# Optimization experiments

Hardware: AMD Instinct MI355X
Metric: run time of the kernel (lower is better)

The kernel has to match this reference:

```python
import jax, jax.numpy as jnp
import numpy as np
from jax import lax


def setup_inputs() -> dict:
    key = jax.random.key(0)
    ks = jax.random.split(key, 3)
    N, Cin, Cout, H, W = 4, 256, 256, 96, 96
    x = jax.random.normal(ks[0], (N, Cin, H, W), jnp.float32)
    # DCNv2-style internal offset/mask conv: 27 = 9 dy + 9 dx + 9 mask logits
    w_off = jax.random.normal(ks[1], (27, Cin, 3, 3), jnp.float32) * 0.01
    b_off = jnp.zeros((27,), jnp.float32)
    w = jax.random.normal(ks[2], (Cout, Cin, 3, 3), jnp.float32) * (1.0 / np.sqrt(Cin * 9))
    b = jnp.zeros((Cout,), jnp.float32)
    gamma = jnp.ones((Cout,), jnp.float32)
    beta = jnp.zeros((Cout,), jnp.float32)
    return {"x": x, "w_off": w_off, "b_off": b_off, "w": w, "b": b, "gamma": gamma, "beta": beta}


def _bilinear(img, py, px):
    # img: [C,H,W]; py,px: [K,H,W] float sampling coords. Zero outside bounds.
    C, H, W = img.shape
    flat = img.reshape(C, -1)
    y0 = jnp.floor(py)
    x0 = jnp.floor(px)
    ly = py - y0
    lx = px - x0

    def gather(yc, xc):
        valid = (yc >= 0) & (yc <= H - 1) & (xc >= 0) & (xc <= W - 1)
        yi = jnp.clip(yc, 0, H - 1).astype(jnp.int32)
        xi = jnp.clip(xc, 0, W - 1).astype(jnp.int32)
        idx = (yi * W + xi).reshape(-1)
        v = flat[:, idx].reshape((C,) + yc.shape)  # [C,K,H,W]
        return v * valid.astype(img.dtype)

    v00 = gather(y0, x0)
    v01 = gather(y0, x0 + 1)
    v10 = gather(y0 + 1, x0)
    v11 = gather(y0 + 1, x0 + 1)
    return (v00 * (1 - ly) * (1 - lx) + v01 * (1 - ly) * lx
            + v10 * ly * (1 - lx) + v11 * ly * lx)


def _forward(x, w_off, b_off, w, b, gamma, beta):
    N, C, H, W = x.shape
    Cout = w.shape[0]
    dn = ("NCHW", "OIHW", "NCHW")
    # internal offset/mask conv (3x3, stride 1, pad 1)
    om = lax.conv_general_dilated(x, w_off, (1, 1), [(1, 1), (1, 1)], dimension_numbers=dn)
    om = om + b_off[None, :, None, None]
    dy, dx, m = om[:, :9], om[:, 9:18], jax.nn.sigmoid(om[:, 18:])
    # base 3x3 kernel grid, dilation 1, padding 1 (centered taps -1..1)
    ky, kx = jnp.meshgrid(jnp.arange(3) - 1, jnp.arange(3) - 1, indexing="ij")
    py = dy + jnp.arange(H, dtype=x.dtype)[None, None, :, None] + ky.reshape(1, 9, 1, 1).astype(x.dtype)
    px = dx + jnp.arange(W, dtype=x.dtype)[None, None, None, :] + kx.reshape(1, 9, 1, 1).astype(x.dtype)
    sampled = jax.vmap(_bilinear)(x, py, px)  # [N,C,9,H,W]
    sampled = sampled * m[:, None]            # DCNv2 modulation mask
    y = jnp.einsum("nckhw,ock->nohw", sampled, w.reshape(Cout, C, 9))
    y = y + b[None, :, None, None]
    # BatchNorm2d (training-mode batch statistics) + ReLU
    mean = y.mean(axis=(0, 2, 3))
    var = y.var(axis=(0, 2, 3))
    y = (y - mean[None, :, None, None]) * lax.rsqrt(var[None, :, None, None] + 1e-5)
    y = y * gamma[None, :, None, None] + beta[None, :, None, None]
    return jax.nn.relu(y)


def reference(x, w_off, b_off, w, b, gamma, beta):
    return _forward(x, w_off, b_off, w, b, gamma, beta)
```

## Files before the change

### kernel.cpp

```cpp
#include <hip/hip_runtime.h>
#include <cmath>

#define H 96
#define W 96
#define HW 9216
#define CIN 256
#define COUT 256
#define NB 4
#define NCH 72
#define NGR 36
#define NIV 18

typedef float f32x4 __attribute__((ext_vector_type(4)));
typedef float f32x2 __attribute__((ext_vector_type(2)));
typedef short bf16x8 __attribute__((ext_vector_type(8)));

__device__ __forceinline__ unsigned short f2bf(float f) {
  unsigned int u = __float_as_uint(f);
  u += 0x7fff + ((u >> 16) & 1);
  return (unsigned short)(u >> 16);
}
__device__ __forceinline__ float bf2f(unsigned short u) {
  return __uint_as_float(((unsigned int)u) << 16);
}
__device__ __forceinline__ f32x2 up2(unsigned int u) {
  f32x2 r;
  r.x = __uint_as_float(u << 16);
  r.y = __uint_as_float(u & 0xffff0000u);
  return r;
}
__device__ __forceinline__ unsigned int cvtpk(float lo, float hi) {
  unsigned int r;
  asm("v_cvt_pk_bf16_f32 %0, %1, %2" : "=v"(r) : "v"(lo), "v"(hi));
  return r;
}

__device__ __forceinline__ void bar() {
  asm volatile("s_waitcnt lgkmcnt(0)" ::: "memory");
  __builtin_amdgcn_s_barrier();
  asm volatile("" ::: "memory");
}

__global__ __launch_bounds__(256)
void xt_convert(const float* __restrict__ x, unsigned short* __restrict__ xT) {
  __shared__ unsigned short ls[64][72];
  int tid = threadIdx.x;
  int hwbase = blockIdx.x * 64;
  int cbase  = blockIdx.y * 64;
  int n      = blockIdx.z;

  {
    int cl = tid >> 2, qd = tid & 3;
    const float* src = x + ((size_t)(n * CIN + cbase + cl)) * HW + hwbase + qd * 16;
#pragma unroll
    for (int m = 0; m < 4; ++m) {
      float4 v = *(const float4*)(src + m * 4);
      int hwl = qd * 16 + m * 4;
      ls[hwl + 0][cl] = f2bf(v.x);
      ls[hwl + 1][cl] = f2bf(v.y);
      ls[hwl + 2][cl] = f2bf(v.z);
      ls[hwl + 3][cl] = f2bf(v.w);
    }
  }
  __syncthreads();
  {
    int hw = tid >> 2, part = tid & 3;
    unsigned short* dst = xT + ((size_t)(n * HW + hwbase + hw)) * CIN + cbase + part * 16;
    *(uint4*)(dst + 0) = *(const uint4*)(&ls[hw][part * 16 + 0]);
    *(uint4*)(dst + 8) = *(const uint4*)(&ls[hw][part * 16 + 8]);
  }
}

__global__ __launch_bounds__(256)
void wa_convert(const float* __restrict__ w, unsigned short* __restrict__ Ag) {
  int gid = blockIdx.x * 256 + threadIdx.x;
  int ch = gid >> 10;
  int rest = gid & 1023;
  int ot = rest >> 6, l = rest & 63;
  int o = ot * 16 + (l & 15);
  int k = ch >> 3, cc = ch & 7;
  int cbase = cc * 32 + (l >> 4) * 8;
  unsigned short r[8];
#pragma unroll
  for (int j = 0; j < 8; ++j)
    r[j] = f2bf(w[((size_t)o * CIN + cbase + j) * 9 + k]);
  uint4 pk;
  pk.x = (unsigned int)r[0] | ((unsigned int)r[1] << 16);
  pk.y = (unsigned int)r[2] | ((unsigned int)r[3] << 16);
  pk.z = (unsigned int)r[4] | ((unsigned int)r[5] << 16);
  pk.w = (unsigned int)r[6] | ((unsigned int)r[7] << 16);
  *(uint4*)(Ag + (size_t)gid * 8) = pk;
}

__global__ __launch_bounds__(256)
void wa2_convert(const float* __restrict__ w_off, unsigned short* __restrict__ Ag2) {
  int gid = blockIdx.x * 256 + threadIdx.x;
  int ch = gid >> 7;
  int rest = gid & 127;
  int ot = rest >> 6, l = rest & 63;
  int o = ot * 16 + (l & 15);
  int k = ch >> 3, cc = ch & 7;
  int cbase = cc * 32 + (l >> 4) * 8;
  unsigned short r[8];
#pragma unroll
  for (int j = 0; j < 8; ++j)
    r[j] = (o < 27) ? f2bf(w_off[((size_t)o * CIN + cbase + j) * 9 + k]) : (unsigned short)0;
  uint4 pk;
  pk.x = (unsigned int)r[0] | ((unsigned int)r[1] << 16);
  pk.y = (unsigned int)r[2] | ((unsigned int)r[3] << 16);
  pk.z = (unsigned int)r[4] | ((unsigned int)r[5] << 16);
  pk.w = (unsigned int)r[6] | ((unsigned int)r[7] << 16);
  *(uint4*)(Ag2 + (size_t)gid * 8) = pk;
}

__global__ __launch_bounds__(256, 4)
void offset_gemm(const unsigned short* __restrict__ xT,
                 const unsigned short* __restrict__ Ag2,
                 const float* __restrict__ b_off,
                 float* __restrict__ py, float* __restrict__ px,
                 float* __restrict__ mk) {
  __shared__ int sPos[9][64];
  __shared__ unsigned short sB[2][2][4096];

  int tid = threadIdx.x;
  int wv = tid >> 6, lane = tid & 63, quad = lane >> 4, l16 = lane & 15;
  int pixBase = blockIdx.x * 64;
  int n = blockIdx.y;
  const unsigned short* xTn = xT + (size_t)n * HW * CIN;

  if (tid < 64) {
    int hwp = pixBase + tid;
    int hh = hwp / W, wx = hwp % W;
#pragma unroll
    for (int ty = 0; ty < 3; ++ty) {
#pragma unroll
      for (int tx = 0; tx < 3; ++tx) {
        int iy = hh + ty - 1, ix = wx + tx - 1;
        bool ok = (iy >= 0) && (iy < H) && (ix >= 0) && (ix < W);
        sPos[ty * 3 + tx][tid] = ok ? (iy * W + ix) : -1;
      }
    }
  }
  bar();

  int pix0 = tid >> 3, ck0 = tid & 7;
  int pix1 = 32 + (tid >> 3);
  int a0 = (ck0 >> 2) * 2048 + (pix0 >> 4) * 512 + ((ck0 & 3) * 16 + ((pix0 & 15) ^ (ck0 & 3))) * 8;
  int a1 = (ck0 >> 2) * 2048 + (pix1 >> 4) * 512 + ((ck0 & 3) * 16 + ((pix1 & 15) ^ (ck0 & 3))) * 8;

  f32x4 acc[2];
  acc[0] = (f32x4){0.f, 0.f, 0.f, 0.f};
  acc[1] = (f32x4){0.f, 0.f, 0.f, 0.f};

  uint4 dA[2], dB[2];
  auto issue = [&](int g, uint4* d) {
    int k = g % 9, c2 = g / 9;
    int p0 = sPos[k][pix0], p1 = sPos[k][pix1];
    d[0] = (uint4){0, 0, 0, 0};
    d[1] = (uint4){0, 0, 0, 0};
    if (p0 >= 0) d[0] = *(const uint4*)(xTn + (size_t)p0 * CIN + c2 * 64 + ck0 * 8);
    if (p1 >= 0) d[1] = *(const uint4*)(xTn + (size_t)p1 * CIN + c2 * 64 + ck0 * 8);
  };

  bf16x8 afr[4];
  auto aload = [&](int g) {
    int k = g % 9, c2 = g / 9;
    int ch = k * 8 + c2 * 2;
#pragma unroll
    for (int s = 0; s < 2; ++s)
#pragma unroll
      for (int ot = 0; ot < 2; ++ot)
        afr[s * 2 + ot] = *(const bf16x8*)(Ag2 + ((size_t)((ch + s) * 2 + ot) * 64 + lane) * 8);
  };

  int rdAddr0 = wv * 512 + (quad * 16 + (l16 ^ quad)) * 8;
  auto mfmaPhase = [&](int buf, int half) {
    const unsigned short* base = &sB[buf][half][0];
    __builtin_amdgcn_s_setprio(1);
#pragma unroll
    for (int s = 0; s < 2; ++s) {
      bf16x8 bfr = *(const bf16x8*)(base + s * 2048 + rdAddr0);
      acc[0] = __builtin_amdgcn_mfma_f32_16x16x32_bf16(afr[s * 2 + 0], bfr, acc[0], 0, 0, 0);
      acc[1] = __builtin_amdgcn_mfma_f32_16x16x32_bf16(afr[s * 2 + 1], bfr, acc[1], 0, 0, 0);
    }
    __builtin_amdgcn_s_setprio(0);
  };
  auto store = [&](uint4* d, int buf, int half) {
    *(uint4*)(&sB[buf][half][a0]) = d[0];
    *(uint4*)(&sB[buf][half][a1]) = d[1];
  };

  issue(0, dA);
  issue(1, dB);
  aload(0);
  store(dA, 0, 0);
  issue(2, dA);
  store(dB, 0, 1);
  issue(3, dB);
  bar();

  for (int i = 0; i < NIV; ++i) {
    int buf = i & 1;
    mfmaPhase(buf, 0);
    aload(2 * i + 1);
    if (i < NIV - 1) store(dA, buf ^ 1, 0);
    if (i < NIV - 2) issue(2 * i + 4, dA);
    mfmaPhase(buf, 1);
    if (i < NIV - 1) store(dB, buf ^ 1, 1);
    if (i < NIV - 2) issue(2 * i + 5, dB);
    if (i < NIV - 1) aload(2 * i + 2);
    bar();
  }

  int pix = pixBase + wv * 16 + l16;
  int he = pix / W, we = pix % W;
#pragma unroll
  for (int ot = 0; ot < 2; ++ot) {
#pragma unroll
    for (int r = 0; r < 4; ++r) {
      int kk = ot * 16 + quad * 4 + r;
      if (kk >= 27) continue;
      float v = acc[ot][r] + b_off[kk];
      if (kk < 9) {
        py[(size_t)(n * 9 + kk) * HW + pix] = v + (float)he + (float)(kk / 3 - 1);
      } else if (kk < 18) {
        int j = kk - 9;
        px[(size_t)(n * 9 + j) * HW + pix] = v + (float)we + (float)(j % 3 - 1);
      } else {
        mk[(size_t)(n * 9 + (kk - 18)) * HW + pix] = 1.f / (1.f + expf(-v));
      }
    }
  }
}

__global__ __launch_bounds__(512, 4)
void fused_gemm(const unsigned short* __restrict__ xT,
                const unsigned short* __restrict__ Ag,
                const float* __restrict__ py,
                const float* __restrict__ px,
                const float* __restrict__ mk,
                unsigned short* __restrict__ yb,
                float* __restrict__ sumArr, float* __restrict__ sqArr) {
  __shared__ int   sIdx4[9][64][4];
  __shared__ float sWgt4[9][64][4];
  __shared__ unsigned short sB[2][2][4096];

  int tid = threadIdx.x;
  int wv = tid >> 6, lane = tid & 63, quad = lane >> 4, l16 = lane & 15;
  int pixBase = blockIdx.x * 64;
  int n = blockIdx.y;
  const unsigned short* xTn = xT + (size_t)n * HW * CIN;

  {
    int pix0 = tid & 63;
    int k0 = tid >> 6;
#pragma unroll
    for (int rep = 0; rep < 2; ++rep) {
      int k = (rep == 0) ? k0 : 8;
      if (rep == 1 && tid >= 64) break;
      int off = (n * 9 + k) * HW + pixBase + pix0;
      float fy = py[off], fx = px[off], fm = mk[off];
      float y0f = floorf(fy), x0f = floorf(fx);
      float ly = fy - y0f, lx = fx - x0f;
      int y0 = (int)y0f, x0 = (int)x0f;
      int cy0 = min(max(y0, 0), H - 1), cy1 = min(max(y0 + 1, 0), H - 1);
      int cx0 = min(max(x0, 0), W - 1), cx1 = min(max(x0 + 1, 0), W - 1);
      float vy0 = (y0 >= 0 && y0 <= H - 1) ? 1.f : 0.f;
      float vy1 = (y0 + 1 >= 0 && y0 + 1 <= H - 1) ? 1.f : 0.f;
      float vx0 = (x0 >= 0 && x0 <= W - 1) ? 1.f : 0.f;
      float vx1 = (x0 + 1 >= 0 && x0 + 1 <= W - 1) ? 1.f : 0.f;
      int4 iv;
      iv.x = cy0 * W + cx0;
      iv.y = cy0 * W + cx1;
      iv.z = cy1 * W + cx0;
      iv.w = cy1 * W + cx1;
      float4 wf;
      wf.x = (1.f - ly) * (1.f - lx) * fm * vy0 * vx0;
      wf.y = (1.f - ly) * lx * fm * vy0 * vx1;
      wf.z = ly * (1.f - lx) * fm * vy1 * vx0;
      wf.w = ly * lx * fm * vy1 * vx1;
      *(int4*)(&sIdx4[k][pix0][0]) = iv;
      *(float4*)(&sWgt4[k][pix0][0]) = wf;
    }
  }
  bar();

  int pixS  = ((wv & 3) << 4) | (lane >> 2);
  int qS    = lane & 3;
  int chunk = ((wv >> 2) << 2) | qS;
  int co    = chunk * 8;
  int sAddr = (chunk >> 2) * 2048 + (wv & 3) * 512 + (qS * 16 + ((lane >> 2) ^ qS)) * 8;

  f32x4 acc[2][4];
#pragma unroll
  for (int i = 0; i < 2; ++i)
#pragma unroll
    for (int pt = 0; pt < 4; ++pt) acc[i][pt] = (f32x4){0.f, 0.f, 0.f, 0.f};

  uint4 cnA[4], cnB[4];
  float wgA[4], wgB[4];
  auto issue = [&](int g, uint4* cn, float* wt) {
    int k = g % 9, c2 = g / 9;
    int4 iv = *(const int4*)(&sIdx4[k][pixS][0]);
    float4 wf = *(const float4*)(&sWgt4[k][pixS][0]);
    int coff = c2 * 64 + co;
    cn[0] = *(const uint4*)(xTn + (size_t)iv.x * CIN + coff);
    cn[1] = *(const uint4*)(xTn + (size_t)iv.y * CIN + coff);
    cn[2] = *(const uint4*)(xTn + (size_t)iv.z * CIN + coff);
    cn[3] = *(const uint4*)(xTn + (size_t)iv.w * CIN + coff);
    wt[0] = wf.x; wt[1] = wf.y; wt[2] = wf.z; wt[3] = wf.w;
  };

  auto blendOne = [&](unsigned int u0, unsigned int u1, unsigned int u2,
                      unsigned int u3, const float* wt) -> unsigned int {
    f32x2 s = up2(u0) * wt[0];
    s += up2(u1) * wt[1];
    s += up2(u2) * wt[2];
    s += up2(u3) * wt[3];
    return cvtpk(s.x, s.y);
  };
  auto blendStore = [&](uint4* cn, const float* wt, int buf, int half) {
    uint4 r;
    r.x = blendOne(cn[0].x, cn[1].x, cn[2].x, cn[3].x, wt);
    r.y = blendOne(cn[0].y, cn[1].y, cn[2].y, cn[3].y, wt);
    r.z = blendOne(cn[0].z, cn[1].z, cn[2].z, cn[3].z, wt);
    r.w = blendOne(cn[0].w, cn[1].w, cn[2].w, cn[3].w, wt);
    *(uint4*)(&sB[buf][half][sAddr]) = r;
  };

  bf16x8 afr[4];
  auto aload = [&](int g) {
    int k = g % 9, c2 = g / 9;
    int ch = k * 8 + c2 * 2;
#pragma unroll
    for (int s = 0; s < 2; ++s)
#pragma unroll
      for (int ot = 0; ot < 2; ++ot)
        afr[s * 2 + ot] = *(const bf16x8*)(Ag + ((size_t)((ch + s) * 16 + 2 * wv + ot) * 64 + lane) * 8);
  };

  int rdBase = (quad * 16 + (l16 ^ quad)) * 8;
  auto mfmaPhase = [&](int buf, int half) {
    const unsigned short* base = &sB[buf][half][0];
    __builtin_amdgcn_s_setprio(1);
#pragma unroll
    for (int s = 0; s < 2; ++s) {
      bf16x8 bfr[4];
#pragma unroll
      for (int pt = 0; pt < 4; ++pt)
        bfr[pt] = *(const bf16x8*)(base + s * 2048 + pt * 512 + rdBase);
#pragma unroll
      for (int pt = 0; pt < 4; ++pt) {
        acc[0][pt] = __builtin_amdgcn_mfma_f32_16x16x32_bf16(afr[s * 2 + 0], bfr[pt], acc[0][pt], 0, 0, 0);
        acc[1][pt] = __builtin_amdgcn_mfma_f32_16x16x32_bf16(afr[s * 2 + 1], bfr[pt], acc[1][pt], 0, 0, 0);
      }
    }
    __builtin_amdgcn_s_setprio(0);
  };

  issue(0, cnA, wgA);
  issue(1, cnB, wgB);
  aload(0);
  blendStore(cnA, wgA, 0, 0);
  issue(2, cnA, wgA);
  blendStore(cnB, wgB, 0, 1);
  issue(3, cnB, wgB);
  bar();

  for (int i = 0; i < NIV; ++i) {
    int buf = i & 1;
    mfmaPhase(buf, 0);
    aload(2 * i + 1);
    if (i < NIV - 1) blendStore(cnA, wgA, buf ^ 1, 0);
    if (i < NIV - 2) issue(2 * i + 4, cnA, wgA);
    mfmaPhase(buf, 1);
    if (i < NIV - 1) blendStore(cnB, wgB, buf ^ 1, 1);
    if (i < NIV - 2) issue(2 * i + 5, cnB, wgB);
    if (i < NIV - 1) aload(2 * i + 2);
    bar();
  }

#pragma unroll
  for (int ot = 0; ot < 2; ++ot) {
#pragma unroll
    for (int r = 0; r < 4; ++r) {
      int o = (2 * wv + ot) * 16 + quad * 4 + r;
      unsigned short* rowp = yb + (size_t)(n * COUT + o) * HW + pixBase;
      float s = 0.f, q = 0.f;
#pragma unroll
      for (int pt = 0; pt < 4; ++pt) {
        float v = acc[ot][pt][r];
        rowp[pt * 16 + l16] = f2bf(v);
        s += v;
        q = fmaf(v, v, q);
      }
#pragma unroll
      for (int m = 8; m >= 1; m >>= 1) {
        s += __shfl_xor(s, m, 64);
        q += __shfl_xor(q, m, 64);
      }
      if (l16 == 0) {
        atomicAdd(&sumArr[o], s);
        atomicAdd(&sqArr[o], q);
      }
    }
  }
}

__global__ __launch_bounds__(256)
void bn_finalize(const float* __restrict__ sumArr, const float* __restrict__ sqArr,
                 const float* __restrict__ gamma, const float* __restrict__ beta,
                 float* __restrict__ scaleArr, float* __restrict__ shiftArr) {
  int o = threadIdx.x;
  const float inv = 1.f / (float)(NB * HW);
  float mean = sumArr[o] * inv;
  float var = sqArr[o] * inv - mean * mean;
  float sc = rsqrtf(var + 1e-5f) * gamma[o];
  scaleArr[o] = sc;
  shiftArr[o] = beta[o] - mean * sc;
}

__global__ __launch_bounds__(256)
void bn_apply(const unsigned short* __restrict__ yb,
              float* __restrict__ out,
              const float* __restrict__ scaleArr,
              const float* __restrict__ shiftArr) {
  int gid = blockIdx.x * 256 + threadIdx.x;
  int base = gid * 8;
  int o = (base / HW) % COUT;
  float scale = scaleArr[o], shift = shiftArr[o];
  uint4 v = ((const uint4*)yb)[gid];
  float4 a, b;
  a.x = fmaxf(fmaf(bf2f((unsigned short)(v.x & 0xffff)), scale, shift), 0.f);
  a.y = fmaxf(fmaf(bf2f((unsigned short)(v.x >> 16)), scale, shift), 0.f);
  a.z = fmaxf(fmaf(bf2f((unsigned short)(v.y & 0xffff)), scale, shift), 0.f);
  a.w = fmaxf(fmaf(bf2f((unsigned short)(v.y >> 16)), scale, shift), 0.f);
  b.x = fmaxf(fmaf(bf2f((unsigned short)(v.z & 0xffff)), scale, shift), 0.f);
  b.y = fmaxf(fmaf(bf2f((unsigned short)(v.z >> 16)), scale, shift), 0.f);
  b.z = fmaxf(fmaf(bf2f((unsigned short)(v.w & 0xffff)), scale, shift), 0.f);
  b.w = fmaxf(fmaf(bf2f((unsigned short)(v.w >> 16)), scale, shift), 0.f);
  *(float4*)&out[base] = a;
  *(float4*)&out[base + 4] = b;
}

extern "C" void kernel_launch(void* const* d_in, const int* in_sizes, int n_in,
                              void* d_out, int out_size, void* d_ws, size_t ws_size,
                              hipStream_t stream) {
  const float* x     = (const float*)d_in[0];
  const float* w_off = (const float*)d_in[1];
  const float* b_off = (const float*)d_in[2];
  const float* w     = (const float*)d_in[3];
  const float* gamma = (const float*)d_in[5];
  const float* beta  = (const float*)d_in[6];
  float* out = (float*)d_out;

  float* ws = (float*)d_ws;
  float* py = ws;
  float* px = py + 331776;
  float* mk = px + 331776;
  unsigned short* Ag  = (unsigned short*)(mk + 331776);
  unsigned short* Ag2 = Ag + 589824;
  float* sumArr   = (float*)(Ag2 + 73728);
  float* sqArr    = sumArr + 256;
  float* scaleArr = sqArr + 256;
  float* shiftArr = scaleArr + 256;
  unsigned short* yb = (unsigned short*)(shiftArr + 256);
  unsigned short* xT = yb + 9437184;

  hipMemsetAsync(sumArr, 0, 512 * sizeof(float), stream);

  dim3 gT(HW / 64, CIN / 64, NB);
  xt_convert<<<gT, 256, 0, stream>>>(x, xT);

  wa_convert<<<(NCH * 16 * 64) / 256, 256, 0, stream>>>(w, Ag);
  wa2_convert<<<(NCH * 2 * 64) / 256, 256, 0, stream>>>(w_off, Ag2);

  dim3 gO(HW / 64, NB);
  offset_gemm<<<gO, 256, 0, stream>>>(xT, Ag2, b_off, py, px, mk);

  dim3 gG(HW / 64, NB);
  fused_gemm<<<gG, 512, 0, stream>>>(xT, Ag, py, px, mk, yb, sumArr, sqArr);

  bn_finalize<<<1, 256, 0, stream>>>(sumArr, sqArr, gamma, beta, scaleArr, shiftArr);
  bn_apply<<<(NB * COUT * HW / 8) / 256, 256, 0, stream>>>(yb, out, scaleArr, shiftArr);
}
```

Baseline: 258.5 us.

## Fuse offset/mask conv GEMM into the deformable GEMM kernel via shared memory

Merges the offset/mask convolution kernel into the main deformable-sampling GEMM kernel. The 27 offset/mask channels for the block's 64 pixels are computed first with 4 of the 8 waves issuing MFMAs, while all 512 threads help stage tiles. The results stay in shared memory instead of round-tripping py/px/mk through global memory. This removes a kernel launch and the global traffic, at the cost of more shared memory per block and four waves idling during the offset phase.

```diff
diff --git a/kernel.cpp b/kernel.cpp
--- a/kernel.cpp
+++ b/kernel.cpp
@@ -113,13 +113,17 @@
   *(uint4*)(Ag2 + (size_t)gid * 8) = pk;
 }
 
-__global__ __launch_bounds__(256, 4)
-void offset_gemm(const unsigned short* __restrict__ xT,
+__global__ __launch_bounds__(512, 4)
+void merged_gemm(const unsigned short* __restrict__ xT,
+                 const unsigned short* __restrict__ Ag,
                  const unsigned short* __restrict__ Ag2,
                  const float* __restrict__ b_off,
-                 float* __restrict__ py, float* __restrict__ px,
-                 float* __restrict__ mk) {
-  __shared__ int sPos[9][64];
+                 unsigned short* __restrict__ yb,
+                 float* __restrict__ sumArr, float* __restrict__ sqArr) {
+  __shared__ int   sPos[9][64];
+  __shared__ float pymk[27][64];
+  __shared__ int   sIdx4[9][64][4];
+  __shared__ float sWgt4[9][64][4];
   __shared__ unsigned short sB[2][2][4096];
 
   int tid = threadIdx.x;
@@ -143,113 +147,95 @@
   }
   bar();
 
-  int pix0 = tid >> 3, ck0 = tid & 7;
-  int pix1 = 32 + (tid >> 3);
-  int a0 = (ck0 >> 2) * 2048 + (pix0 >> 4) * 512 + ((ck0 & 3) * 16 + ((pix0 & 15) ^ (ck0 & 3))) * 8;
-  int a1 = (ck0 >> 2) * 2048 + (pix1 >> 4) * 512 + ((ck0 & 3) * 16 + ((pix1 & 15) ^ (ck0 & 3))) * 8;
-
-  f32x4 acc[2];
-  acc[0] = (f32x4){0.f, 0.f, 0.f, 0.f};
-  acc[1] = (f32x4){0.f, 0.f, 0.f, 0.f};
-
-  uint4 dA[2], dB[2];
-  auto issue = [&](int g, uint4* d) {
+  int pixA = tid >> 3, ckA = tid & 7;
+  int aA = (ckA >> 2) * 2048 + (pixA >> 4) * 512 + ((ckA & 3) * 16 + ((pixA & 15) ^ (ckA & 3))) * 8;
+
+  f32x4 accA[2];
+  accA[0] = (f32x4){0.f, 0.f, 0.f, 0.f};
+  accA[1] = (f32x4){0.f, 0.f, 0.f, 0.f};
+
+  uint4 dA, dB;
+  auto issueA = [&](int g, uint4* d) {
     int k = g % 9, c2 = g / 9;
-    int p0 = sPos[k][pix0], p1 = sPos[k][pix1];
-    d[0] = (uint4){0, 0, 0, 0};
-    d[1] = (uint4){0, 0, 0, 0};
-    if (p0 >= 0) d[0] = *(const uint4*)(xTn + (size_t)p0 * CIN + c2 * 64 + ck0 * 8);
-    if (p1 >= 0) d[1] = *(const uint4*)(xTn + (size_t)p1 * CIN + c2 * 64 + ck0 * 8);
-  };
-
-  bf16x8 afr[4];
-  auto aload = [&](int g) {
+    int p = sPos[k][pixA];
+    *d = (uint4){0, 0, 0, 0};
+    if (p >= 0) *d = *(const uint4*)(xTn + (size_t)p * CIN + c2 * 64 + ckA * 8);
+  };
+
+  bf16x8 afrA[4];
+  auto aloadA = [&](int g) {
     int k = g % 9, c2 = g / 9;
     int ch = k * 8 + c2 * 2;
 #pragma unroll
     for (int s = 0; s < 2; ++s)
 #pragma unroll
       for (int ot = 0; ot < 2; ++ot)
-        afr[s * 2 + ot] = *(const bf16x8*)(Ag2 + ((size_t)((ch + s) * 2 + ot) * 64 + lane) * 8);
-  };
-
-  int rdAddr0 = wv * 512 + (quad * 16 + (l16 ^ quad)) * 8;
-  auto mfmaPhase = [&](int buf, int half) {
+        afrA[s * 2 + ot] = *(const bf16x8*)(Ag2 + ((size_t)((ch + s) * 2 + ot) * 64 + lane) * 8);
+  };
+
+  int rdA = wv * 512 + (quad * 16 + (l16 ^ quad)) * 8;
+  auto mfmaA = [&](int buf, int half) {
     const unsigned short* base = &sB[buf][half][0];
     __builtin_amdgcn_s_setprio(1);
 #pragma unroll
     for (int s = 0; s < 2; ++s) {
-      bf16x8 bfr = *(const bf16x8*)(base + s * 2048 + rdAddr0);
-      acc[0] = __builtin_amdgcn_mfma_f32_16x16x32_bf16(afr[s * 2 + 0], bfr, acc[0], 0, 0, 0);
-      acc[1] = __builtin_amdgcn_mfma_f32_16x16x32_bf16(afr[s * 2 + 1], bfr, acc[1], 0, 0, 0);
+      bf16x8 bfr = *(const bf16x8*)(base + s * 2048 + rdA);
+      accA[0] = __builtin_amdgcn_mfma_f32_16x16x32_bf16(afrA[s * 2 + 0], bfr, accA[0], 0, 0, 0);
+      accA[1] = __builtin_amdgcn_mfma_f32_16x16x32_bf16(afrA[s * 2 + 1], bfr, accA[1], 0, 0, 0);
     }
     __builtin_amdgcn_s_setprio(0);
   };
-  auto store = [&](uint4* d, int buf, int half) {
-    *(uint4*)(&sB[buf][half][a0]) = d[0];
-    *(uint4*)(&sB[buf][half][a1]) = d[1];
-  };
-
-  issue(0, dA);
-  issue(1, dB);
-  aload(0);
-  store(dA, 0, 0);
-  issue(2, dA);
-  store(dB, 0, 1);
-  issue(3, dB);
+  auto storeA = [&](uint4 d, int buf, int half) {
+    *(uint4*)(&sB[buf][half][aA]) = d;
+  };
+
+  issueA(0, &dA);
+  issueA(1, &dB);
+  if (wv < 4) aloadA(0);
+  storeA(dA, 0, 0);
+  issueA(2, &dA);
+  storeA(dB, 0, 1);
+  issueA(3, &dB);
   bar();
 
   for (int i = 0; i < NIV; ++i) {
     int buf = i & 1;
-    mfmaPhase(buf, 0);
-    aload(2 * i + 1);
-    if (i < NIV - 1) store(dA, buf ^ 1, 0);
-    if (i < NIV - 2) issue(2 * i + 4, dA);
-    mfmaPhase(buf, 1);
-    if (i < NIV - 1) store(dB, buf ^ 1, 1);
-    if (i < NIV - 2) issue(2 * i + 5, dB);
-    if (i < NIV - 1) aload(2 * i + 2);
+    if (wv < 4) {
+      mfmaA(buf, 0);
+      aloadA(2 * i + 1);
+    }
+    if (i < NIV - 1) storeA(dA, buf ^ 1, 0);
+    if (i < NIV - 2) issueA(2 * i + 4, &dA);
+    if (wv < 4) mfmaA(buf, 1);
+    if (i < NIV - 1) storeA(dB, buf ^ 1, 1);
+    if (i < NIV - 2) issueA(2 * i + 5, &dB);
+    if (i < NIV - 1 && wv < 4) aloadA(2 * i + 2);
     bar();
   }
 
-  int pix = pixBase + wv * 16 + l16;
-  int he = pix / W, we = pix % W;
-#pragma unroll
-  for (int ot = 0; ot < 2; ++ot) {
-#pragma unroll
-    for (int r = 0; r < 4; ++r) {
-      int kk = ot * 16 + quad * 4 + r;
-      if (kk >= 27) continue;
-      float v = acc[ot][r] + b_off[kk];
-      if (kk < 9) {
-        py[(size_t)(n * 9 + kk) * HW + pix] = v + (float)he + (float)(kk / 3 - 1);
-      } else if (kk < 18) {
-        int j = kk - 9;
-        px[(size_t)(n * 9 + j) * HW + pix] = v + (float)we + (float)(j % 3 - 1);
-      } else {
-        mk[(size_t)(n * 9 + (kk - 18)) * HW + pix] = 1.f / (1.f + expf(-v));
-      }
-    }
-  }
-}
-
-__global__ __launch_bounds__(512, 4)
-void fused_gemm(const unsigned short* __restrict__ xT,
-                const unsigned short* __restrict__ Ag,
-                const float* __restrict__ py,
-                const float* __restrict__ px,
-                const float* __restrict__ mk,
-                unsigned short* __restrict__ yb,
-                float* __restrict__ sumArr, float* __restrict__ sqArr) {
-  __shared__ int   sIdx4[9][64][4];
-  __shared__ float sWgt4[9][64][4];
-  __shared__ unsigned short sB[2][2][4096];
-
-  int tid = threadIdx.x;
-  int wv = tid >> 6, lane = tid & 63, quad = lane >> 4, l16 = lane & 15;
-  int pixBase = blockIdx.x * 64;
-  int n = blockIdx.y;
-  const unsigned short* xTn = xT + (size_t)n * HW * CIN;
+  if (wv < 4) {
+    int pixL = wv * 16 + l16;
+    int pixG = pixBase + pixL;
+    int he = pixG / W, we = pixG % W;
+#pragma unroll
+    for (int ot = 0; ot < 2; ++ot) {
+#pragma unroll
+      for (int r = 0; r < 4; ++r) {
+        int kk = ot * 16 + quad * 4 + r;
+        if (kk >= 27) continue;
+        float v = accA[ot][r] + b_off[kk];
+        if (kk < 9) {
+          pymk[kk][pixL] = v + (float)he + (float)(kk / 3 - 1);
+        } else if (kk < 18) {
+          int j = kk - 9;
+          pymk[kk][pixL] = v + (float)we + (float)(j % 3 - 1);
+        } else {
+          pymk[kk][pixL] = 1.f / (1.f + expf(-v));
+        }
+      }
+    }
+  }
+  bar();
 
   {
     int pix0 = tid & 63;
@@ -258,8 +244,7 @@
     for (int rep = 0; rep < 2; ++rep) {
       int k = (rep == 0) ? k0 : 8;
       if (rep == 1 && tid >= 64) break;
-      int off = (n * 9 + k) * HW + pixBase + pix0;
-      float fy = py[off], fx = px[off], fm = mk[off];
+      float fy = pymk[k][pix0], fx = pymk[9 + k][pix0], fm = pymk[18 + k][pix0];
       float y0f = floorf(fy), x0f = floorf(fx);
       float ly = fy - y0f, lx = fx - x0f;
       int y0 = (int)y0f, x0 = (int)x0f;
@@ -454,11 +439,7 @@
   const float* beta  = (const float*)d_in[6];
   float* out = (float*)d_out;
 
-  float* ws = (float*)d_ws;
-  float* py = ws;
-  float* px = py + 331776;
-  float* mk = px + 331776;
-  unsigned short* Ag  = (unsigned short*)(mk + 331776);
+  unsigned short* Ag  = (unsigned short*)d_ws;
   unsigned short* Ag2 = Ag + 589824;
   float* sumArr   = (float*)(Ag2 + 73728);
   float* sqArr    = sumArr + 256;
@@ -475,11 +456,8 @@
   wa_convert<<<(NCH * 16 * 64) / 256, 256, 0, stream>>>(w, Ag);
   wa2_convert<<<(NCH * 2 * 64) / 256, 256, 0, stream>>>(w_off, Ag2);
 
-  dim3 gO(HW / 64, NB);
-  offset_gemm<<<gO, 256, 0, stream>>>(xT, Ag2, b_off, py, px, mk);
-
-  dim3 gG(HW / 64, NB);
-  fused_gemm<<<gG, 512, 0, stream>>>(xT, Ag, py, px, mk, yb, sumArr, sqArr);
+  dim3 gM(HW / 64, NB);
+  merged_gemm<<<gM, 512, 0, stream>>>(xT, Ag, Ag2, b_off, yb, sumArr, sqArr);
 
   bn_finalize<<<1, 256, 0, stream>>>(sumArr, sqArr, gamma, beta, scaleArr, shiftArr);
   bn_apply<<<(NB * COUT * HW / 8) / 256, 256, 0, stream>>>(yb, out, scaleArr, shiftArr);
```

New measurement: 265.7 us. +2.8%, slower.
